# Kernel tuning notes

Measured on AMD Instinct MI355X. Metric: run time of the kernel, lower is better.

Reference implementation:

```python
import jax, jax.numpy as jnp
import numpy as np

B, H, L, D = 4, 4096, 8, 64  # queries shape [B, L, H, D]
FACTOR = 5
U = FACTOR * int(np.ceil(np.log(4096)))  # u_part = u = 45 (L_q == L_k)


def setup_inputs() -> dict:
    key = jax.random.key(0)
    kq, kk, kv, ki = jax.random.split(key, 4)
    queries = jax.random.normal(kq, (4, 4096, 8, 64), dtype=jnp.float32)
    keys = jax.random.normal(kk, (4, 4096, 8, 64), dtype=jnp.float32)
    values = jax.random.normal(kv, (4, 4096, 8, 64), dtype=jnp.float32)
    index_sample = jax.random.randint(ki, (4096, U), 0, 4096)  # torch.randint(key_length,(L_Q,sample_k))
    return {"queries": queries, "keys": keys, "values": values, "index_sample": index_sample}


def reference(queries, keys, values, index_sample):
    # (B, L, H, D) -> (B, H, L, D)
    q = jnp.transpose(queries, (0, 2, 1, 3))
    k = jnp.transpose(keys, (0, 2, 1, 3))
    v = jnp.transpose(values, (0, 2, 1, 3))
    b, h, l_q, d = q.shape
    l_k = k.shape[2]
    n_top = index_sample.shape[1]  # u == u_part == 45 here

    # --- _prob_QK: sampled QK scores (avoid materializing key_expand [B,H,Lq,Lk,D]) ---
    # key_sample: [B, H, Lq, sample_k, D]
    key_sample = k[:, :, index_sample, :]
    # Q_i . K_sampled: [B, H, Lq, sample_k]
    qk_sample = jnp.einsum('bhld,bhlsd->bhls', q, key_sample)
    # sparsity measure M = max - mean(over full key_length)
    m = jnp.max(qk_sample, axis=-1) - jnp.sum(qk_sample, axis=-1) / l_k  # [B,H,Lq]
    _, m_top = jax.lax.top_k(m, n_top)  # [B, H, u]

    # reduced queries: [B, H, u, D]
    q_reduce = jnp.take_along_axis(q, m_top[..., None], axis=2)
    scores_top = jnp.einsum('bhud,bhkd->bhuk', q_reduce, k)  # [B, H, u, Lk]

    scale = 1.0 / jnp.sqrt(jnp.asarray(d, dtype=q.dtype))
    scores_top = scores_top * scale

    # --- _get_initial_context (mask_flag=False): mean of values broadcast over queries ---
    context = jnp.broadcast_to(jnp.mean(v, axis=2, keepdims=True), (b, h, l_q, d))

    # --- _update_context: softmax + scatter attn@V into the top-u query rows ---
    attn = jax.nn.softmax(scores_top, axis=-1)  # [B, H, u, Lk]
    update = jnp.einsum('bhuk,bhkd->bhud', attn, v)  # [B, H, u, D]
    b_idx = jnp.arange(b)[:, None, None]
    h_idx = jnp.arange(h)[None, :, None]
    context = context.at[b_idx, h_idx, m_top].set(update)
    return context  # [B, H, Lq, D]
```

## Files before the change

kernel.cpp:

```cpp
#include <hip/hip_runtime.h>
#include <hip/hip_bf16.h>


#define NB 4
#define NH 8
#define NL 4096
#define ND 64
#define NS 45
#define SCALE 0.125f
#define NCHUNK 16
#define CHUNK 256

typedef float floatx4 __attribute__((ext_vector_type(4)));

static __device__ __forceinline__ float neg_inf() { return -__builtin_inff(); }

template <int CTRL>
static __device__ __forceinline__ float dpp_add(float x) {
  int y = __builtin_amdgcn_update_dpp(0, __builtin_bit_cast(int, x), CTRL,
                                      0xF, 0xF, true);
  return x + __builtin_bit_cast(float, y);
}
static __device__ __forceinline__ float red16(float x) {
  x = dpp_add<0x140>(x);
  x = dpp_add<0x141>(x);
  x = dpp_add<0x4E>(x);
  x = dpp_add<0xB1>(x);
  return x;
}
static __device__ __forceinline__ float red4(float x) {
  x = dpp_add<0xB1>(x);
  x = dpp_add<0x4E>(x);
  return x;
}

__global__ __launch_bounds__(256) void kA_m_meanv(
    const float* __restrict__ q, const float* __restrict__ k,
    const float* __restrict__ v, const int* __restrict__ idxs,
    float* __restrict__ m_out, float* __restrict__ vpart)
{
  __shared__ int sidx[4][48];
  __shared__ float part[4][ND];
  int gb = blockIdx.x;
  int t = threadIdx.x, w = t >> 6, lane = t & 63, g = lane >> 4;

  if (gb < 8192) {
    int pair = gb & 7;
    int b = pair >> 1, hg = pair & 1;
    int lg = gb >> 3;
    int l = lg * 4 + w;

    if (lane < NS) sidx[w][lane] = idxs[l * NS + lane];

    const floatx4* q4 =
        (const floatx4*)(q + ((size_t)(b * NL + l) * NH + hg * 4) * ND);
    floatx4 qr = __builtin_nontemporal_load(q4 + lane);
    const float* kbase = k + ((size_t)b * NL * NH + hg * 4) * ND;

    float mx = neg_inf(), sm = 0.f;
#pragma unroll 1
    for (int s0 = 0; s0 < NS; s0 += 9) {
      floatx4 kr[9];
#pragma unroll
      for (int j = 0; j < 9; j++) {
        int ki = __builtin_amdgcn_readfirstlane(sidx[w][s0 + j]);
        kr[j] = *((const floatx4*)(kbase + (size_t)ki * 512) + lane);
      }
      float p[9];
#pragma unroll
      for (int j = 0; j < 9; j++) {
        float d = kr[j].x * qr.x + kr[j].y * qr.y + kr[j].z * qr.z +
                  kr[j].w * qr.w;
        p[j] = red16(d);
      }
      float m0 = fmaxf(fmaxf(p[0], p[1]), p[2]);
      float m1 = fmaxf(fmaxf(p[3], p[4]), p[5]);
      float m2 = fmaxf(fmaxf(p[6], p[7]), p[8]);
      mx = fmaxf(fmaxf(mx, m0), fmaxf(m1, m2));
      sm += ((p[0] + p[1]) + (p[2] + p[3])) +
            ((p[4] + p[5]) + (p[6] + p[7])) + p[8];
    }
    if ((lane & 15) == 0)
      m_out[((size_t)b * NH + hg * 4 + g) * NL + l] = mx - sm * (1.0f / 4096.0f);
  } else {
    int idx = gb - 8192;
    int bh = idx >> 6, c = idx & 63;
    int b = bh >> 3, h = bh & 7;
    int d = t & 63, gg = t >> 6;
    float a0 = 0.f, a1 = 0.f, a2 = 0.f, a3 = 0.f;
    const float* vb = v + ((size_t)(b * NL + c * 64) * NH + h) * ND + d;
#pragma unroll
    for (int i = 0; i < 4; i++) {
      a0 += vb[(size_t)(gg + 4 * (4 * i + 0)) * NH * ND];
      a1 += vb[(size_t)(gg + 4 * (4 * i + 1)) * NH * ND];
      a2 += vb[(size_t)(gg + 4 * (4 * i + 2)) * NH * ND];
      a3 += vb[(size_t)(gg + 4 * (4 * i + 3)) * NH * ND];
    }
    part[gg][d] = (a0 + a1) + (a2 + a3);
    __syncthreads();
    if (gg == 0) {
      float s = part[0][d] + part[1][d] + part[2][d] + part[3][d];
      vpart[(bh * 64 + c) * ND + d] = s;
    }
  }
}

__global__ __launch_bounds__(256) void k_topk_p1(
    const float* __restrict__ m_in, unsigned long long* __restrict__ cand)
{
  __shared__ unsigned long long keys[512];
  __shared__ unsigned long long wred[4];
  int blk = blockIdx.x;
  int bh = blk >> 3, slice = blk & 7;
  int t = threadIdx.x, wid = t >> 6, lane = t & 63;
  int base = slice * 512;
  for (int i = t; i < 512; i += 256) {
    float v = m_in[bh * NL + base + i];
    unsigned u = __float_as_uint(v);
    u ^= (u >> 31) ? 0xFFFFFFFFu : 0x80000000u;
    keys[i] = ((unsigned long long)u << 32) | (unsigned)(~(unsigned)(base + i));
  }
  __syncthreads();
  for (int it = 0; it < NS; ++it) {
    unsigned long long k0 = keys[t], k1 = keys[t + 256];
    unsigned long long best = k0 > k1 ? k0 : k1;
#pragma unroll
    for (int off = 32; off; off >>= 1) {
      unsigned long long o = __shfl_xor(best, off);
      if (o > best) best = o;
    }
    if (lane == 0) wred[wid] = best;
    __syncthreads();
    if (t == 0) {
      unsigned long long b0 = wred[0];
      if (wred[1] > b0) b0 = wred[1];
      if (wred[2] > b0) b0 = wred[2];
      if (wred[3] > b0) b0 = wred[3];
      cand[blk * NS + it] = b0;
      int gi = (int)(~(unsigned)(b0 & 0xFFFFFFFFull));
      keys[gi - base] = 0;
    }
    __syncthreads();
  }
}

__global__ __launch_bounds__(256) void kC_topk2_meanv(
    const unsigned long long* __restrict__ cand, int* __restrict__ mtop,
    const float* __restrict__ vpart, float* __restrict__ meanv)
{
  __shared__ unsigned long long keys[8 * NS];
  __shared__ unsigned long long wred[4];
  __shared__ unsigned long long sbest;
  __shared__ float part2[4][ND];
  int gb = blockIdx.x;
  int t = threadIdx.x, wid = t >> 6, lane = t & 63;

  if (gb < 32) {
    int bh = gb;
    for (int i = t; i < 8 * NS; i += 256) keys[i] = cand[bh * 8 * NS + i];
    __syncthreads();
    for (int it = 0; it < NS; ++it) {
      unsigned long long best = (t < 8 * NS) ? keys[t] : 0ull;
      if (t + 256 < 8 * NS) {
        unsigned long long k1 = keys[t + 256];
        if (k1 > best) best = k1;
      }
#pragma unroll
      for (int off = 32; off; off >>= 1) {
        unsigned long long o = __shfl_xor(best, off);
        if (o > best) best = o;
      }
      if (lane == 0) wred[wid] = best;
      __syncthreads();
      if (t == 0) {
        unsigned long long b0 = wred[0];
        if (wred[1] > b0) b0 = wred[1];
        if (wred[2] > b0) b0 = wred[2];
        if (wred[3] > b0) b0 = wred[3];
        sbest = b0;
        mtop[bh * NS + it] = (int)(~(unsigned)(b0 & 0xFFFFFFFFull));
      }
      __syncthreads();
      unsigned long long bb = sbest;
      if (t < 8 * NS && keys[t] == bb) keys[t] = 0;
      if (t + 256 < 8 * NS && keys[t + 256] == bb) keys[t + 256] = 0;
      __syncthreads();
    }
  } else {
    int bh = gb - 32;
    int d = t & 63, gg = t >> 6;
    float s = 0.f;
#pragma unroll
    for (int i = 0; i < 16; i++) s += vpart[(bh * 64 + gg + 4 * i) * ND + d];
    part2[gg][d] = s;
    __syncthreads();
    if (gg == 0) {
      float tot = part2[0][d] + part2[1][d] + part2[2][d] + part2[3][d];
      meanv[bh * ND + d] = tot * (1.0f / 4096.0f);
    }
  }
}

__global__ __launch_bounds__(1024) void kD_scores_fill(
    const float* __restrict__ q, const float* __restrict__ k,
    const float* __restrict__ v, const int* __restrict__ mtop,
    const float* __restrict__ meanv,
    float* __restrict__ mc_out, float* __restrict__ lc_out,
    float* __restrict__ op_out, float* __restrict__ out)
{
  __shared__ float QLDS[NS * ND];
  __shared__ float SLDS[NS * 260];
  __shared__ int mt[NS];
  __shared__ float mcs[NS], lcs[NS];

  int gb = blockIdx.x;
  int t = threadIdx.x;
  int wid = t >> 6, lane = t & 63;

  if (gb >= 512) {
    const int total = NB * NH * NL * ND / 4;
    const floatx4* mv4 = (const floatx4*)meanv;
    floatx4* o4 = (floatx4*)out;
    for (int i = (gb - 512) * 1024 + t; i < total; i += 512 * 1024) {
      int bh = i >> 16;
      __builtin_nontemporal_store(mv4[bh * 16 + (i & 15)], o4 + i);
    }
    return;
  }

  int xcd = gb & 7, seq = gb >> 3;
  int bh = xcd * 4 + (seq >> 4);
  int c = seq & 15;
  int b = bh >> 3, h = bh & 7;

  if (t < NS) mt[t] = mtop[bh * NS + t];
  __syncthreads();

  const float4* q4 = (const float4*)q;
  float4* QL4 = (float4*)QLDS;
  if (t < NS * 16) {
    int u = t >> 4, j = t & 15;
    QL4[t] = q4[((size_t)(b * NL + mt[u]) * NH + h) * 16 + j];
  }
  __syncthreads();

  {
    int wh = wid & 7;
    int kk = wh * 16 + (lane >> 2);
    int seg = lane & 3;
    int u0 = (wid < 8) ? 0 : 23;
    int u1 = (wid < 8) ? 23 : NS;
    const float4* kA4 =
        (const float4*)(k + ((size_t)(b * NL + c * CHUNK + kk) * NH + h) * ND)
        + seg * 4;
    const float4* kB4 =
        (const float4*)(k + ((size_t)(b * NL + c * CHUNK + kk + 128) * NH + h) * ND)
        + seg * 4;
    float4 ka0 = kA4[0], ka1 = kA4[1], ka2 = kA4[2], ka3 = kA4[3];
    float4 kb0 = kB4[0], kb1 = kB4[1], kb2 = kB4[2], kb3 = kB4[3];
    const float4* qp = QL4 + seg * 4;
    for (int u = u0; u < u1; ++u) {
      float4 a0 = qp[u * 16 + 0], a1 = qp[u * 16 + 1];
      float4 a2 = qp[u * 16 + 2], a3 = qp[u * 16 + 3];
      float dA = a0.x * ka0.x + a0.y * ka0.y + a0.z * ka0.z + a0.w * ka0.w
               + a1.x * ka1.x + a1.y * ka1.y + a1.z * ka1.z + a1.w * ka1.w
               + a2.x * ka2.x + a2.y * ka2.y + a2.z * ka2.z + a2.w * ka2.w
               + a3.x * ka3.x + a3.y * ka3.y + a3.z * ka3.z + a3.w * ka3.w;
      float dB = a0.x * kb0.x + a0.y * kb0.y + a0.z * kb0.z + a0.w * kb0.w
               + a1.x * kb1.x + a1.y * kb1.y + a1.z * kb1.z + a1.w * kb1.w
               + a2.x * kb2.x + a2.y * kb2.y + a2.z * kb2.z + a2.w * kb2.w
               + a3.x * kb3.x + a3.y * kb3.y + a3.z * kb3.z + a3.w * kb3.w;
      dA = red4(dA);
      dB = red4(dB);
      if (seg == 0) {
        SLDS[u * 260 + kk] = dA * SCALE;
        SLDS[u * 260 + kk + 128] = dB * SCALE;
      }
    }
  }
  __syncthreads();

  for (int u = wid; u < NS; u += 16) {
    float4 sv = *(const float4*)&SLDS[u * 260 + lane * 4];
    float mx = fmaxf(fmaxf(sv.x, sv.y), fmaxf(sv.z, sv.w));
#pragma unroll
    for (int off = 32; off; off >>= 1) mx = fmaxf(mx, __shfl_xor(mx, off));
    float e0 = expf(sv.x - mx), e1 = expf(sv.y - mx);
    float e2 = expf(sv.z - mx), e3 = expf(sv.w - mx);
    float s = e0 + e1 + e2 + e3;
#pragma unroll
    for (int off = 32; off; off >>= 1) s += __shfl_xor(s, off);
    *(float4*)&SLDS[u * 260 + lane * 4] = make_float4(e0, e1, e2, e3);
    if (lane == 0) { mcs[u] = mx; lcs[u] = s; }
  }
  __syncthreads();

  float acc[3];
#pragma unroll
  for (int i = 0; i < 3; i++) acc[i] = 0.f;
  const float* vbase = v + ((size_t)(b * NL + c * CHUNK) * NH + h) * ND + lane;
  for (int kb = 0; kb < 64; ++kb) {
    float vd0 = vbase[(size_t)(kb * 4 + 0) * NH * ND];
    float vd1 = vbase[(size_t)(kb * 4 + 1) * NH * ND];
    float vd2 = vbase[(size_t)(kb * 4 + 2) * NH * ND];
    float vd3 = vbase[(size_t)(kb * 4 + 3) * NH * ND];
#pragma unroll
    for (int i = 0; i < 3; i++) {
      int u = wid + 16 * i;
      if (u < NS) {
        float4 p4 = *(const float4*)&SLDS[u * 260 + kb * 4];
        acc[i] += p4.x * vd0 + p4.y * vd1 + p4.z * vd2 + p4.w * vd3;
      }
    }
  }
#pragma unroll
  for (int i = 0; i < 3; i++) {
    int u = wid + 16 * i;
    if (u < NS)
      op_out[(((size_t)bh * NCHUNK + c) * NS + u) * ND + lane] = acc[i];
  }
  if (t < NS) {
    mc_out[(bh * NCHUNK + c) * NS + t] = mcs[t];
    lc_out[(bh * NCHUNK + c) * NS + t] = lcs[t];
  }
}

__global__ __launch_bounds__(256) void k_combine(
    const float* __restrict__ mc, const float* __restrict__ lc,
    const float* __restrict__ op, const int* __restrict__ mtop,
    float* __restrict__ out)
{
  int gw = blockIdx.x * 4 + (threadIdx.x >> 6);
  int lane = threadIdx.x & 63;
  int bh = gw / NS, u = gw % NS;
  float M = neg_inf();
  for (int c = 0; c < NCHUNK; c++)
    M = fmaxf(M, mc[(bh * NCHUNK + c) * NS + u]);
  float Lsum = 0.f, O = 0.f;
  for (int c = 0; c < NCHUNK; c++) {
    float e = expf(mc[(bh * NCHUNK + c) * NS + u] - M);
    Lsum += lc[(bh * NCHUNK + c) * NS + u] * e;
    O += op[(((size_t)bh * NCHUNK + c) * NS + u) * ND + lane] * e;
  }
  int row = mtop[bh * NS + u];
  out[((size_t)bh * NL + row) * ND + lane] = O / Lsum;
}

extern "C" void kernel_launch(void* const* d_in, const int* in_sizes, int n_in,
                              void* d_out, int out_size, void* d_ws, size_t ws_size,
                              hipStream_t stream) {
  const float* q = (const float*)d_in[0];
  const float* k = (const float*)d_in[1];
  const float* v = (const float*)d_in[2];
  const int* idxs = (const int*)d_in[3];
  float* out = (float*)d_out;
  float* ws = (float*)d_ws;

  float* m_ws  = ws;
  int*   mtop  = (int*)(ws + 131072);
  float* meanv = ws + 132512;
  float* mc    = ws + 134560;
  float* lc    = ws + 157600;
  float* op    = ws + 180640;
  float* vpart = op;
  unsigned long long* cand = (unsigned long long*)(op + 131072);

  hipLaunchKernelGGL(kA_m_meanv,     dim3(8192 + 2048), dim3(256),  0, stream,
                     q, k, v, idxs, m_ws, vpart);
  hipLaunchKernelGGL(k_topk_p1,      dim3(256),         dim3(256),  0, stream,
                     m_ws, cand);
  hipLaunchKernelGGL(kC_topk2_meanv, dim3(64),          dim3(256),  0, stream,
                     cand, mtop, vpart, meanv);
  hipLaunchKernelGGL(kD_scores_fill, dim3(1024),        dim3(1024), 0, stream,
                     q, k, v, mtop, meanv, mc, lc, op, out);
  hipLaunchKernelGGL(k_combine,      dim3(360),         dim3(256),  0, stream,
                     mc, lc, op, mtop, out);
}
```

Baseline: 175.4 us.

## Split P·V across key-groups with LDS reduction to reuse V loads

Reorganizes the attn@V phase so each wave handles a quarter of the chunk's keys and 12 query rows, instead of all 256 keys and up to 3 query rows. Each V element loaded from global memory is now reused across 12 queries rather than 3, so each wave issues fewer global loads. The four partial sums are reduced serially through LDS with extra barriers, and the output is written as float4. The cost is more registers per thread and several extra __syncthreads.

After: 172.9 us, median of 2. About the same (-1.4%).

```diff
diff --git a/kernel.cpp b/kernel.cpp
--- a/kernel.cpp
+++ b/kernel.cpp
@@ -295,29 +295,48 @@
   }
   __syncthreads();
 
-  float acc[3];
-#pragma unroll
-  for (int i = 0; i < 3; i++) acc[i] = 0.f;
-  const float* vbase = v + ((size_t)(b * NL + c * CHUNK) * NH + h) * ND + lane;
-  for (int kb = 0; kb < 64; ++kb) {
-    float vd0 = vbase[(size_t)(kb * 4 + 0) * NH * ND];
-    float vd1 = vbase[(size_t)(kb * 4 + 1) * NH * ND];
-    float vd2 = vbase[(size_t)(kb * 4 + 2) * NH * ND];
-    float vd3 = vbase[(size_t)(kb * 4 + 3) * NH * ND];
-#pragma unroll
-    for (int i = 0; i < 3; i++) {
-      int u = wid + 16 * i;
-      if (u < NS) {
-        float4 p4 = *(const float4*)&SLDS[u * 260 + kb * 4];
-        acc[i] += p4.x * vd0 + p4.y * vd1 + p4.z * vd2 + p4.w * vd3;
-      }
-    }
-  }
-#pragma unroll
-  for (int i = 0; i < 3; i++) {
-    int u = wid + 16 * i;
-    if (u < NS)
-      op_out[(((size_t)bh * NCHUNK + c) * NS + u) * ND + lane] = acc[i];
+  {
+    int kg = wid & 3, ug = wid >> 2;
+    float acc[12];
+#pragma unroll
+    for (int i = 0; i < 12; i++) acc[i] = 0.f;
+    const float* vbase =
+        v + ((size_t)(b * NL + c * CHUNK + kg * 64) * NH + h) * ND + lane;
+    const float* prow = &SLDS[kg * 64];
+    for (int kb = 0; kb < 16; ++kb) {
+      float vd0 = vbase[(size_t)(kb * 4 + 0) * NH * ND];
+      float vd1 = vbase[(size_t)(kb * 4 + 1) * NH * ND];
+      float vd2 = vbase[(size_t)(kb * 4 + 2) * NH * ND];
+      float vd3 = vbase[(size_t)(kb * 4 + 3) * NH * ND];
+#pragma unroll
+      for (int i = 0; i < 12; i++) {
+        int u = ug * 12 + i;
+        if (u < NS) {
+          float4 p4 = *(const float4*)&prow[u * 260 + kb * 4];
+          acc[i] += p4.x * vd0 + p4.y * vd1 + p4.z * vd2 + p4.w * vd3;
+        }
+      }
+    }
+    __syncthreads();
+#pragma unroll
+    for (int r = 0; r < 4; ++r) {
+      if (kg == r) {
+#pragma unroll
+        for (int i = 0; i < 12; i++) {
+          int u = ug * 12 + i;
+          if (u < NS) {
+            if (r == 0) QLDS[u * ND + lane] = acc[i];
+            else        QLDS[u * ND + lane] += acc[i];
+          }
+        }
+      }
+      __syncthreads();
+    }
+  }
+
+  if (t < NS * 16) {
+    float4* op4 = (float4*)(op_out + (((size_t)bh * NCHUNK + c) * NS) * ND);
+    op4[t] = QL4[t];
   }
   if (t < NS) {
     mc_out[(bh * NCHUNK + c) * NS + t] = mcs[t];
```
